# Performance work log

Measured on AMD Instinct MI355X. Metric: run time of the kernel, lower is better.

## Reference

```python
import jax, jax.numpy as jnp
import numpy as np

N_NODES = 100000
N_EDGES = 3200000
IN_DIM = 128
HID = 128
K = 20  # n_gaussians


def gcn_conv(x, src, dst, W, b, n_nodes):
    """PyG GCNConv: add self-loops, symmetric normalization, linear transform.
    out = D^{-1/2} (A + I) D^{-1/2} (x @ W) + b, where D is degree of A+I.
    """
    h = x @ W  # [N, out_dim]
    # degree on A + I (self-loop contributes 1 to every node)
    deg = jax.ops.segment_sum(jnp.ones_like(dst, dtype=h.dtype), dst,
                              num_segments=n_nodes) + 1.0
    dis = jax.lax.rsqrt(deg)  # deg >= 1, safe
    norm = dis[src] * dis[dst]  # [E]
    # gather -> scale -> scatter-add (edges), plus self-loop term dis_i^2 * h_i
    agg = jax.ops.segment_sum(h[src] * norm[:, None], dst,
                              num_segments=n_nodes)
    agg = agg + h * (dis * dis)[:, None]
    return agg + b


def setup_inputs() -> dict:
    key = jax.random.key(0)
    ks = jax.random.split(key, 12)
    x = jax.random.normal(ks[0], (N_NODES, IN_DIM), dtype=jnp.float32)
    edge_index = jax.random.randint(ks[1], (2, N_EDGES), 0, N_NODES, dtype=jnp.int32)
    s = 1.0 / np.sqrt(HID)
    W1 = jax.random.uniform(ks[2], (IN_DIM, HID), jnp.float32, -s, s)
    b1 = jnp.zeros((HID,), jnp.float32)
    W2 = jax.random.uniform(ks[3], (HID, HID), jnp.float32, -s, s)
    b2 = jnp.zeros((HID,), jnp.float32)
    pi_W = jax.random.uniform(ks[4], (HID, K), jnp.float32, -s, s)
    pi_b = jnp.zeros((K,), jnp.float32)
    mu_W = jax.random.uniform(ks[5], (HID, K), jnp.float32, -s, s)
    mu_b = jnp.zeros((K,), jnp.float32)
    ls_W = jax.random.uniform(ks[6], (HID, K), jnp.float32, -s, s)
    ls_b = jnp.zeros((K,), jnp.float32)
    return {"x": x, "edge_index": edge_index, "W1": W1, "b1": b1,
            "W2": W2, "b2": b2, "pi_W": pi_W, "pi_b": pi_b,
            "mu_W": mu_W, "mu_b": mu_b, "ls_W": ls_W, "ls_b": ls_b}


def reference(x, edge_index, W1, b1, W2, b2, pi_W, pi_b, mu_W, mu_b, ls_W, ls_b):
    src, dst = edge_index[0], edge_index[1]
    n = x.shape[0]
    h = jax.nn.relu(gcn_conv(x, src, dst, W1, b1, n))
    h = jax.nn.relu(gcn_conv(h, src, dst, W2, b2, n))
    pi = jax.nn.softmax(h @ pi_W + pi_b, axis=1)
    mu = h @ mu_W + mu_b
    log_sigma = h @ ls_W + ls_b
    return (pi, mu, log_sigma)
```

## Files before the change

### kernel.cpp

```cpp
#include <hip/hip_runtime.h>
#include <hip/hip_fp16.h>
#include <cstdint>
#include <cstddef>

#define IN_DIM 128
#define HID    128
#define NG     20
#define T      4096
#define MAXB   400

__global__ void zero_ints(int* __restrict__ a, int n) {
  int i = blockIdx.x * blockDim.x + threadIdx.x;
  if (i < n) a[i] = 0;
}

__global__ __launch_bounds__(256) void binsort1(const int* __restrict__ src,
    const int* __restrict__ dst, int* __restrict__ tmp, int* __restrict__ bofs,
    int* __restrict__ bintot, int NBC, int E) {
  __shared__ int lhist[MAXB];
  __shared__ int lscan[512];
  __shared__ int lcur[MAXB];
  __shared__ int sbuf[T];
  int tid = threadIdx.x;
  int tile0 = blockIdx.x * T;
  int m = E - tile0; if (m > T) m = T;

  for (int i = tid; i < NBC; i += 256) lhist[i] = 0;
  __syncthreads();

  int dreg[16];
#pragma unroll
  for (int j = 0; j < 16; ++j) {
    int idx = j * 256 + tid;
    dreg[j] = -1;
    if (idx < m) {
      int d = dst[tile0 + idx];
      dreg[j] = d;
      atomicAdd(&lhist[d >> 8], 1);
    }
  }
  __syncthreads();

  int v0 = (tid < NBC) ? lhist[tid] : 0;
  int v1 = (256 + tid < NBC) ? lhist[256 + tid] : 0;
  lscan[tid] = v0; lscan[256 + tid] = v1;
  __syncthreads();
  for (int o = 1; o < 512; o <<= 1) {
    int a0 = (tid >= o) ? lscan[tid - o] : 0;
    int a1 = (256 + tid >= o) ? lscan[256 + tid - o] : 0;
    __syncthreads();
    lscan[tid] += a0; lscan[256 + tid] += a1;
    __syncthreads();
  }
  if (tid < NBC)       lcur[tid]       = lscan[tid] - v0;
  if (256 + tid < NBC) lcur[256 + tid] = lscan[256 + tid] - v1;
  __syncthreads();

  int ST = NBC + 1;
  for (int i = tid; i < NBC; i += 256) bofs[(size_t)blockIdx.x * ST + i] = lcur[i];
  if (tid == 0) bofs[(size_t)blockIdx.x * ST + NBC] = m;
  for (int i = tid; i < NBC; i += 256)
    if (lhist[i]) atomicAdd(&bintot[i], lhist[i]);
  __syncthreads();

#pragma unroll
  for (int j = 0; j < 16; ++j) {
    int idx = j * 256 + tid;
    if (idx < m) {
      int d = dreg[j];
      int s = src[tile0 + idx];
      int slot = atomicAdd(&lcur[d >> 8], 1);
      sbuf[slot] = ((d & 255) << 17) | s;
    }
  }
  __syncthreads();

  int nv = m >> 2;
  int4* out4 = (int4*)(tmp + tile0);
  const int4* sb4 = (const int4*)sbuf;
  for (int i = tid; i < nv; i += 256) out4[i] = sb4[i];
  for (int i = (nv << 2) + tid; i < m; i += 256) tmp[tile0 + i] = sbuf[i];
}

__global__ __launch_bounds__(512) void binscan(const int* __restrict__ bintot,
                                               int* __restrict__ binbase, int NBC) {
  __shared__ int s[512];
  int tid = threadIdx.x;
  int v = (tid < NBC) ? bintot[tid] : 0;
  s[tid] = v;
  __syncthreads();
  for (int o = 1; o < 512; o <<= 1) {
    int t = (tid >= o) ? s[tid - o] : 0;
    __syncthreads();
    s[tid] += t;
    __syncthreads();
  }
  if (tid < NBC) binbase[tid] = s[tid] - v;
}

__global__ __launch_bounds__(512) void binsort2(const int* __restrict__ tmp,
    const int* __restrict__ bofs, const int* __restrict__ binbase,
    int* __restrict__ csrc, int* __restrict__ cnt, float* __restrict__ dis,
    int* __restrict__ offs, int NBC, int nblk, int N) {
  __shared__ int lcnt[256];
  __shared__ int lsc[256];
  __shared__ int lcur2[256];
  int b = blockIdx.x;
  int tid = threadIdx.x;
  if (tid < 256) lcnt[tid] = 0;
  __syncthreads();
  int ST = NBC + 1;
  for (int r = tid; r < nblk; r += 512) {
    int s = bofs[(size_t)r * ST + b];
    int e2 = bofs[(size_t)r * ST + b + 1];
    int base = r * T;
    for (int k = s; k < e2; ++k)
      atomicAdd(&lcnt[tmp[base + k] >> 17], 1);
  }
  __syncthreads();
  if (tid < 256) lsc[tid] = lcnt[tid];
  __syncthreads();
  for (int o = 1; o < 256; o <<= 1) {
    int t = 0;
    if (tid < 256 && tid >= o) t = lsc[tid - o];
    __syncthreads();
    if (tid < 256) lsc[tid] += t;
    __syncthreads();
  }
  int gbase = binbase[b];
  if (tid < 256) {
    int excl = lsc[tid] - lcnt[tid];
    lcur2[tid] = gbase + excl;
    int node = (b << 8) + tid;
    if (node < N) {
      cnt[node] = lcnt[tid];
      dis[node] = rsqrtf((float)lcnt[tid] + 1.0f);
      offs[node] = gbase + excl;
    }
  }
  __syncthreads();
  for (int r = tid; r < nblk; r += 512) {
    int s = bofs[(size_t)r * ST + b];
    int e2 = bofs[(size_t)r * ST + b + 1];
    int base = r * T;
    for (int k = s; k < e2; ++k) {
      int rec = tmp[base + k];
      int pos = atomicAdd(&lcur2[rec >> 17], 1);
      csrc[pos] = rec & 0x1FFFF;
    }
  }
}

#define MT 64
#define KC 64
__global__ __launch_bounds__(256) void gemm128_f16out(const float* __restrict__ A,
                                                      const float* __restrict__ B,
                                                      __half* __restrict__ C, int M) {
  __shared__ float sA[MT][KC + 4];
  __shared__ float sB[KC][128];
  int tid = threadIdx.x;
  int m0 = blockIdx.x * MT;
  int tr = tid >> 4;
  int tc = tid & 15;
  float acc[4][8];
#pragma unroll
  for (int i = 0; i < 4; ++i)
#pragma unroll
    for (int j = 0; j < 8; ++j) acc[i][j] = 0.f;

  for (int k0 = 0; k0 < 128; k0 += KC) {
#pragma unroll
    for (int q = 0; q < 4; ++q) {
      int idx = q * 256 + tid;
      int r = idx >> 4;
      int kk = (idx & 15) << 2;
      float4 v = make_float4(0.f, 0.f, 0.f, 0.f);
      if (m0 + r < M) v = *(const float4*)(A + (size_t)(m0 + r) * 128 + k0 + kk);
      *(float4*)(&sA[r][kk]) = v;
    }
#pragma unroll
    for (int q = 0; q < 8; ++q) {
      int idx = q * 256 + tid;
      int kk = idx >> 5;
      int nn = (idx & 31) << 2;
      *(float4*)(&sB[kk][nn]) = *(const float4*)(B + (size_t)(k0 + kk) * 128 + nn);
    }
    __syncthreads();
#pragma unroll 2
    for (int k = 0; k < KC; k += 4) {
      float4 a0 = *(const float4*)(&sA[tr][k]);
      float4 a1 = *(const float4*)(&sA[tr + 16][k]);
      float4 a2 = *(const float4*)(&sA[tr + 32][k]);
      float4 a3 = *(const float4*)(&sA[tr + 48][k]);
#pragma unroll
      for (int u = 0; u < 4; ++u) {
        float4 blo = *(const float4*)(&sB[k + u][tc * 4]);
        float4 bhi = *(const float4*)(&sB[k + u][64 + tc * 4]);
        float av[4] = {((const float*)&a0)[u], ((const float*)&a1)[u],
                       ((const float*)&a2)[u], ((const float*)&a3)[u]};
        float bl[8] = {blo.x, blo.y, blo.z, blo.w, bhi.x, bhi.y, bhi.z, bhi.w};
#pragma unroll
        for (int i = 0; i < 4; ++i)
#pragma unroll
          for (int j = 0; j < 8; ++j) acc[i][j] = fmaf(av[i], bl[j], acc[i][j]);
      }
    }
    __syncthreads();
  }
#pragma unroll
  for (int i = 0; i < 4; ++i) {
    int r = m0 + tr + 16 * i;
    if (r < M) {
      __half2 p0 = __floats2half2_rn(acc[i][0], acc[i][1]);
      __half2 p1 = __floats2half2_rn(acc[i][2], acc[i][3]);
      __half2 p2 = __floats2half2_rn(acc[i][4], acc[i][5]);
      __half2 p3 = __floats2half2_rn(acc[i][6], acc[i][7]);
      __half2* dst0 = (__half2*)(C + (size_t)r * 128 + tc * 4);
      __half2* dst1 = (__half2*)(C + (size_t)r * 128 + 64 + tc * 4);
      dst0[0] = p0; dst0[1] = p1;
      dst1[0] = p2; dst1[1] = p3;
    }
  }
}

__global__ __launch_bounds__(256) void agg_kernel(const __half* __restrict__ h,
    const int* __restrict__ csrc,
    const int* __restrict__ offs, const int* __restrict__ cnt,
    const float* __restrict__ dis, const float* __restrict__ bias,
    float* __restrict__ out, int n) {
  int wave = threadIdx.x >> 6;
  int lane = threadIdx.x & 63;
  int i0 = (blockIdx.x * 4 + wave) * 2;
  if (i0 >= n) return;
  int i1 = i0 + 1;
  bool has1 = i1 < n;
  int c = lane * 2;

  int st0 = offs[i0];
  int m0  = cnt[i0];
  float d0 = dis[i0];
  int st1 = 0, m1 = 0;
  float d1 = 0.f;
  if (has1) { st1 = offs[i1]; m1 = cnt[i1]; d1 = dis[i1]; }

  float ax0 = 0.f, ay0 = 0.f, ax1 = 0.f, ay1 = 0.f;
  int mMax = m0 > m1 ? m0 : m1;

  for (int base = 0; base < mMax; base += 64) {
    int mcA = m0 - base; mcA = mcA < 0 ? 0 : (mcA > 64 ? 64 : mcA);
    int mcB = m1 - base; mcB = mcB < 0 ? 0 : (mcB > 64 ? 64 : mcB);
    int mc = mcA > mcB ? mcA : mcB;

    int sA = 0, sB = 0;
    float wA = 0.f, wB = 0.f;
    if (lane < mcA) sA = csrc[st0 + base + lane];
    if (lane < mcB) sB = csrc[st1 + base + lane];
    if (lane < mcA) wA = dis[sA] * d0;
    if (lane < mcB) wB = dis[sB] * d1;

    int j = 0;
    for (; j + 4 <= mc; j += 4) {
      int   a0 = __shfl(sA, j);
      int   a1 = __shfl(sA, j + 1);
      int   a2 = __shfl(sA, j + 2);
      int   a3 = __shfl(sA, j + 3);
      int   b0 = __shfl(sB, j);
      int   b1 = __shfl(sB, j + 1);
      int   b2 = __shfl(sB, j + 2);
      int   b3 = __shfl(sB, j + 3);
      float u0 = __shfl(wA, j);
      float u1 = __shfl(wA, j + 1);
      float u2 = __shfl(wA, j + 2);
      float u3 = __shfl(wA, j + 3);
      float v0 = __shfl(wB, j);
      float v1 = __shfl(wB, j + 1);
      float v2 = __shfl(wB, j + 2);
      float v3 = __shfl(wB, j + 3);
      float2 hA0 = __half22float2(*(const __half2*)(h + ((size_t)a0 << 7) + c));
      float2 hA1 = __half22float2(*(const __half2*)(h + ((size_t)a1 << 7) + c));
      float2 hA2 = __half22float2(*(const __half2*)(h + ((size_t)a2 << 7) + c));
      float2 hA3 = __half22float2(*(const __half2*)(h + ((size_t)a3 << 7) + c));
      float2 hB0 = __half22float2(*(const __half2*)(h + ((size_t)b0 << 7) + c));
      float2 hB1 = __half22float2(*(const __half2*)(h + ((size_t)b1 << 7) + c));
      float2 hB2 = __half22float2(*(const __half2*)(h + ((size_t)b2 << 7) + c));
      float2 hB3 = __half22float2(*(const __half2*)(h + ((size_t)b3 << 7) + c));
      ax0 = fmaf(hA0.x, u0, ax0); ay0 = fmaf(hA0.y, u0, ay0);
      ax0 = fmaf(hA1.x, u1, ax0); ay0 = fmaf(hA1.y, u1, ay0);
      ax0 = fmaf(hA2.x, u2, ax0); ay0 = fmaf(hA2.y, u2, ay0);
      ax0 = fmaf(hA3.x, u3, ax0); ay0 = fmaf(hA3.y, u3, ay0);
      ax1 = fmaf(hB0.x, v0, ax1); ay1 = fmaf(hB0.y, v0, ay1);
      ax1 = fmaf(hB1.x, v1, ax1); ay1 = fmaf(hB1.y, v1, ay1);
      ax1 = fmaf(hB2.x, v2, ax1); ay1 = fmaf(hB2.y, v2, ay1);
      ax1 = fmaf(hB3.x, v3, ax1); ay1 = fmaf(hB3.y, v3, ay1);
    }
    for (; j < mc; ++j) {
      int   a0 = __shfl(sA, j);
      int   b0 = __shfl(sB, j);
      float u0 = __shfl(wA, j);
      float v0 = __shfl(wB, j);
      float2 hA0 = __half22float2(*(const __half2*)(h + ((size_t)a0 << 7) + c));
      float2 hB0 = __half22float2(*(const __half2*)(h + ((size_t)b0 << 7) + c));
      ax0 = fmaf(hA0.x, u0, ax0); ay0 = fmaf(hA0.y, u0, ay0);
      ax1 = fmaf(hB0.x, v0, ax1); ay1 = fmaf(hB0.y, v0, ay1);
    }
  }

  float2 bv = *(const float2*)(bias + c);
  {
    float dd = d0 * d0;
    float2 hs = __half22float2(*(const __half2*)(h + ((size_t)i0 << 7) + c));
    float vx = fmaf(hs.x, dd, ax0) + bv.x;
    float vy = fmaf(hs.y, dd, ay0) + bv.y;
    *(float2*)(out + (size_t)i0 * 128 + c) = make_float2(fmaxf(vx, 0.f), fmaxf(vy, 0.f));
  }
  if (has1) {
    float dd = d1 * d1;
    float2 hs = __half22float2(*(const __half2*)(h + ((size_t)i1 << 7) + c));
    float vx = fmaf(hs.x, dd, ax1) + bv.x;
    float vy = fmaf(hs.y, dd, ay1) + bv.y;
    *(float2*)(out + (size_t)i1 * 128 + c) = make_float2(fmaxf(vx, 0.f), fmaxf(vy, 0.f));
  }
}

__global__ void pack_heads_w(const float* __restrict__ piW, const float* __restrict__ muW,
                             const float* __restrict__ lsW, float* __restrict__ W64) {
  int i = blockIdx.x * 256 + threadIdx.x;
  if (i >= 128 * 64) return;
  int k = i >> 6, j = i & 63;
  float v = 0.f;
  if (j < 20)      v = piW[k * 20 + j];
  else if (j < 40) v = muW[k * 20 + (j - 20)];
  else if (j < 60) v = lsW[k * 20 + (j - 40)];
  W64[i] = v;
}

__global__ __launch_bounds__(256) void gemm_heads(const float* __restrict__ A,
                                                  const float* __restrict__ B,
                                                  float* __restrict__ C, int M) {
  __shared__ float sA[64][KC + 4];
  __shared__ float sB[KC][68];
  int tid = threadIdx.x;
  int m0 = blockIdx.x * 64;
  int tr = tid >> 4;
  int tc = tid & 15;
  float acc[4][4];
#pragma unroll
  for (int i = 0; i < 4; ++i)
#pragma unroll
    for (int j = 0; j < 4; ++j) acc[i][j] = 0.f;

  for (int k0 = 0; k0 < 128; k0 += KC) {
#pragma unroll
    for (int q = 0; q < 4; ++q) {
      int idx = q * 256 + tid;
      int r = idx >> 4;
      int kk = (idx & 15) << 2;
      float4 v = make_float4(0.f, 0.f, 0.f, 0.f);
      if (m0 + r < M) v = *(const float4*)(A + (size_t)(m0 + r) * 128 + k0 + kk);
      *(float4*)(&sA[r][kk]) = v;
    }
#pragma unroll
    for (int q = 0; q < 4; ++q) {
      int idx = q * 256 + tid;
      int kk = idx >> 4;
      int nn = (idx & 15) << 2;
      *(float4*)(&sB[kk][nn]) = *(const float4*)(B + (size_t)(k0 + kk) * 64 + nn);
    }
    __syncthreads();
#pragma unroll 4
    for (int k = 0; k < KC; k += 4) {
      float4 a0 = *(const float4*)(&sA[tr][k]);
      float4 a1 = *(const float4*)(&sA[tr + 16][k]);
      float4 a2 = *(const float4*)(&sA[tr + 32][k]);
      float4 a3 = *(const float4*)(&sA[tr + 48][k]);
#pragma unroll
      for (int u = 0; u < 4; ++u) {
        float4 b = *(const float4*)(&sB[k + u][tc * 4]);
        float av[4] = {((const float*)&a0)[u], ((const float*)&a1)[u],
                       ((const float*)&a2)[u], ((const float*)&a3)[u]};
#pragma unroll
        for (int i = 0; i < 4; ++i) {
          acc[i][0] = fmaf(av[i], b.x, acc[i][0]);
          acc[i][1] = fmaf(av[i], b.y, acc[i][1]);
          acc[i][2] = fmaf(av[i], b.z, acc[i][2]);
          acc[i][3] = fmaf(av[i], b.w, acc[i][3]);
        }
      }
    }
    __syncthreads();
  }
#pragma unroll
  for (int i = 0; i < 4; ++i) {
    int r = m0 + tr + 16 * i;
    if (r < M)
      *(float4*)(C + (size_t)r * 64 + tc * 4) =
          make_float4(acc[i][0], acc[i][1], acc[i][2], acc[i][3]);
  }
}

__global__ __launch_bounds__(256) void heads_post(const float* __restrict__ out60,
    const float* __restrict__ pib, const float* __restrict__ mub,
    const float* __restrict__ lsb, float* __restrict__ out, int n) {
  int wave = threadIdx.x >> 6, lane = threadIdx.x & 63;
  int node = blockIdx.x * 4 + wave;
  if (node >= n) return;
  float v = 0.f;
  if (lane < 60) {
    v = out60[(size_t)node * 64 + lane];
    v += (lane < 20) ? pib[lane] : (lane < 40) ? mub[lane - 20] : lsb[lane - 40];
  }
  float pv = (lane < 20) ? v : -__builtin_inff();
  float mx = pv;
  for (int o = 16; o > 0; o >>= 1) mx = fmaxf(mx, __shfl_down(mx, o, 32));
  mx = __shfl(mx, 0, 32);
  float ev = (lane < 20) ? expf(v - mx) : 0.f;
  float sm = ev;
  for (int o = 16; o > 0; o >>= 1) sm += __shfl_down(sm, o, 32);
  sm = __shfl(sm, 0, 32);

  size_t base = (size_t)n * NG;
  if (lane < 20)      out[(size_t)node * NG + lane] = ev / sm;
  else if (lane < 40) out[base + (size_t)node * NG + (lane - 20)] = v;
  else if (lane < 60) out[2 * base + (size_t)node * NG + (lane - 40)] = v;
}

extern "C" void kernel_launch(void* const* d_in, const int* in_sizes, int n_in,
                              void* d_out, int out_size, void* d_ws, size_t ws_size,
                              hipStream_t stream) {
  const float* x   = (const float*)d_in[0];
  const int*   ei  = (const int*)d_in[1];
  const float* W1  = (const float*)d_in[2];
  const float* b1  = (const float*)d_in[3];
  const float* W2  = (const float*)d_in[4];
  const float* b2  = (const float*)d_in[5];
  const float* piW = (const float*)d_in[6];
  const float* pib = (const float*)d_in[7];
  const float* muW = (const float*)d_in[8];
  const float* mub = (const float*)d_in[9];
  const float* lsW = (const float*)d_in[10];
  const float* lsb = (const float*)d_in[11];
  float* out = (float*)d_out;

  const int N = in_sizes[0] / IN_DIM;
  const int E = in_sizes[1] / 2;
  const int* src = ei;
  const int* dst = ei + E;

  const int NBC  = (N + 255) >> 8;
  const int nblk = (E + T - 1) / T;
  const int ST   = NBC + 1;

  char* p = (char*)d_ws;
  char* regionH = p;                        p += (size_t)N * HID * sizeof(__half);
  __half* h16  = (__half*)regionH;
  float* out60 = (float*)regionH;
  char* regionR = p;
  size_t szR = (size_t)N * HID * sizeof(float);
  size_t szT = (size_t)E * sizeof(int);
  p += (szR > szT ? szR : szT);
  int*   tmp    = (int*)regionR;
  float* bufB   = (float*)regionR;
  int*   csrc   = (int*)p;                  p += (size_t)E * sizeof(int);
  int*   bofs   = (int*)p;                  p += (size_t)nblk * ST * sizeof(int);
  int*   bintot = (int*)p;                  p += (size_t)MAXB * sizeof(int);
  int*   binbase= (int*)p;                  p += (size_t)MAXB * sizeof(int);
  int*   cnt    = (int*)p;                  p += (size_t)N * sizeof(int);
  int*   offs   = (int*)p;                  p += (size_t)N * sizeof(int);
  float* dis    = (float*)p;                p += (size_t)N * sizeof(float);
  float* W64    = (float*)p;                p += (size_t)128 * 64 * sizeof(float);

  zero_ints<<<(NBC + 255) / 256, 256, 0, stream>>>(bintot, NBC);
  binsort1<<<nblk, 256, 0, stream>>>(src, dst, tmp, bofs, bintot, NBC, E);
  binscan<<<1, 512, 0, stream>>>(bintot, binbase, NBC);
  binsort2<<<NBC, 512, 0, stream>>>(tmp, bofs, binbase, csrc, cnt, dis, offs,
                                    NBC, nblk, N);
  pack_heads_w<<<(128 * 64 + 255) / 256, 256, 0, stream>>>(piW, muW, lsW, W64);

  const int NB8 = (N + 7) / 8;

  gemm128_f16out<<<(N + MT - 1) / MT, 256, 0, stream>>>(x, W1, h16, N);
  agg_kernel<<<NB8, 256, 0, stream>>>(h16, csrc, offs, cnt, dis, b1, bufB, N);
  gemm128_f16out<<<(N + MT - 1) / MT, 256, 0, stream>>>(bufB, W2, h16, N);
  agg_kernel<<<NB8, 256, 0, stream>>>(h16, csrc, offs, cnt, dis, b2, bufB, N);

  gemm_heads<<<(N + 63) / 64, 256, 0, stream>>>(bufB, W64, out60, N);
  heads_post<<<(N + 3) / 4, 256, 0, stream>>>(out60, pib, mub, lsb, out, N);
}
```

Baseline: 591.2 us.

## Fuse aggregation with following dense transform and heads epilogue

Layer-1 aggregation now computes the 8 aggregated rows per block into shared memory and immediately multiplies them by W2, writing fp16 h directly, eliminating the fp32 intermediate round trip and a separate GEMM launch. The second aggregation likewise fuses the heads GEMM and softmax/split epilogue, removing two kernels and the out60 buffer. The tradeoff is that the fused GEMMs read W from global/L2 per block with little reuse (8 rows per block, no shared tiling of W), so compute efficiency of the dense part drops.

```diff
diff --git a/kernel.cpp b/kernel.cpp
--- a/kernel.cpp
+++ b/kernel.cpp
@@ -223,29 +223,12 @@
   }
 }
 
-__global__ __launch_bounds__(256) void agg_kernel(const __half* __restrict__ h,
-    const int* __restrict__ csrc,
-    const int* __restrict__ offs, const int* __restrict__ cnt,
-    const float* __restrict__ dis, const float* __restrict__ bias,
-    float* __restrict__ out, int n) {
-  int wave = threadIdx.x >> 6;
+__device__ __forceinline__ void agg_core(const __half* __restrict__ h,
+    const int* __restrict__ csrc, const float* __restrict__ dis,
+    int st0, int m0, float d0, int st1, int m1, float d1, int c,
+    float& ax0, float& ay0, float& ax1, float& ay1) {
   int lane = threadIdx.x & 63;
-  int i0 = (blockIdx.x * 4 + wave) * 2;
-  if (i0 >= n) return;
-  int i1 = i0 + 1;
-  bool has1 = i1 < n;
-  int c = lane * 2;
-
-  int st0 = offs[i0];
-  int m0  = cnt[i0];
-  float d0 = dis[i0];
-  int st1 = 0, m1 = 0;
-  float d1 = 0.f;
-  if (has1) { st1 = offs[i1]; m1 = cnt[i1]; d1 = dis[i1]; }
-
-  float ax0 = 0.f, ay0 = 0.f, ax1 = 0.f, ay1 = 0.f;
   int mMax = m0 > m1 ? m0 : m1;
-
   for (int base = 0; base < mMax; base += 64) {
     int mcA = m0 - base; mcA = mcA < 0 ? 0 : (mcA > 64 ? 64 : mcA);
     int mcB = m1 - base; mcB = mcB < 0 ? 0 : (mcB > 64 ? 64 : mcB);
@@ -304,21 +287,161 @@
       ax1 = fmaf(hB0.x, v0, ax1); ay1 = fmaf(hB0.y, v0, ay1);
     }
   }
-
-  float2 bv = *(const float2*)(bias + c);
+}
+
+__global__ __launch_bounds__(256) void agg_gemm_h(const __half* __restrict__ h,
+    const int* __restrict__ csrc, const int* __restrict__ offs,
+    const int* __restrict__ cnt, const float* __restrict__ dis,
+    const float* __restrict__ bias, const float* __restrict__ W,
+    __half* __restrict__ outH, int n) {
+  __shared__ float sRow[8][128];
+  const int tid = threadIdx.x;
+  const int wave = tid >> 6, lane = tid & 63;
+  const int n0 = blockIdx.x * 8;
+  const int i0 = n0 + wave * 2;
+  const int i1 = i0 + 1;
+  const int c = lane * 2;
+
+  if (i0 < n) {
+    const bool has1 = i1 < n;
+    int st0 = offs[i0];
+    int m0  = cnt[i0];
+    float d0 = dis[i0];
+    int st1 = 0, m1 = 0;
+    float d1 = 0.f;
+    if (has1) { st1 = offs[i1]; m1 = cnt[i1]; d1 = dis[i1]; }
+    float ax0 = 0.f, ay0 = 0.f, ax1 = 0.f, ay1 = 0.f;
+    agg_core(h, csrc, dis, st0, m0, d0, st1, m1, d1, c, ax0, ay0, ax1, ay1);
+
+    float2 bv = *(const float2*)(bias + c);
+    {
+      float dd = d0 * d0;
+      float2 hs = __half22float2(*(const __half2*)(h + ((size_t)i0 << 7) + c));
+      sRow[wave * 2][c]     = fmaxf(fmaf(hs.x, dd, ax0) + bv.x, 0.f);
+      sRow[wave * 2][c + 1] = fmaxf(fmaf(hs.y, dd, ay0) + bv.y, 0.f);
+    }
+    if (has1) {
+      float dd = d1 * d1;
+      float2 hs = __half22float2(*(const __half2*)(h + ((size_t)i1 << 7) + c));
+      sRow[wave * 2 + 1][c]     = fmaxf(fmaf(hs.x, dd, ax1) + bv.x, 0.f);
+      sRow[wave * 2 + 1][c + 1] = fmaxf(fmaf(hs.y, dd, ay1) + bv.y, 0.f);
+    }
+  }
+  __syncthreads();
+
+  const int r = tid >> 5;
+  const int q = tid & 31;
+  float4 acc = make_float4(0.f, 0.f, 0.f, 0.f);
+  const float* wp = W + q * 4;
+#pragma unroll 4
+  for (int k = 0; k < 128; k += 4) {
+    float4 a4 = *(const float4*)(&sRow[r][k]);
+    float4 w0 = *(const float4*)(wp + (size_t)(k + 0) * 128);
+    float4 w1 = *(const float4*)(wp + (size_t)(k + 1) * 128);
+    float4 w2 = *(const float4*)(wp + (size_t)(k + 2) * 128);
+    float4 w3 = *(const float4*)(wp + (size_t)(k + 3) * 128);
+    acc.x = fmaf(a4.x, w0.x, acc.x); acc.y = fmaf(a4.x, w0.y, acc.y);
+    acc.z = fmaf(a4.x, w0.z, acc.z); acc.w = fmaf(a4.x, w0.w, acc.w);
+    acc.x = fmaf(a4.y, w1.x, acc.x); acc.y = fmaf(a4.y, w1.y, acc.y);
+    acc.z = fmaf(a4.y, w1.z, acc.z); acc.w = fmaf(a4.y, w1.w, acc.w);
+    acc.x = fmaf(a4.z, w2.x, acc.x); acc.y = fmaf(a4.z, w2.y, acc.y);
+    acc.z = fmaf(a4.z, w2.z, acc.z); acc.w = fmaf(a4.z, w2.w, acc.w);
+    acc.x = fmaf(a4.w, w3.x, acc.x); acc.y = fmaf(a4.w, w3.y, acc.y);
+    acc.z = fmaf(a4.w, w3.z, acc.z); acc.w = fmaf(a4.w, w3.w, acc.w);
+  }
+  if (n0 + r < n) {
+    __half2 p0 = __floats2half2_rn(acc.x, acc.y);
+    __half2 p1 = __floats2half2_rn(acc.z, acc.w);
+    __half2* dp = (__half2*)(outH + (((size_t)(n0 + r)) << 7) + q * 4);
+    dp[0] = p0; dp[1] = p1;
+  }
+}
+
+__global__ __launch_bounds__(256) void agg_gemm_heads(const __half* __restrict__ h,
+    const int* __restrict__ csrc, const int* __restrict__ offs,
+    const int* __restrict__ cnt, const float* __restrict__ dis,
+    const float* __restrict__ bias, const float* __restrict__ W64,
+    const float* __restrict__ pib, const float* __restrict__ mub,
+    const float* __restrict__ lsb, float* __restrict__ out, int n) {
+  __shared__ float sRow[8][128];
+  __shared__ float sOut[8][64];
+  const int tid = threadIdx.x;
+  const int wave = tid >> 6, lane = tid & 63;
+  const int n0 = blockIdx.x * 8;
+  const int i0 = n0 + wave * 2;
+  const int i1 = i0 + 1;
+  const int c = lane * 2;
+
+  if (i0 < n) {
+    const bool has1 = i1 < n;
+    int st0 = offs[i0];
+    int m0  = cnt[i0];
+    float d0 = dis[i0];
+    int st1 = 0, m1 = 0;
+    float d1 = 0.f;
+    if (has1) { st1 = offs[i1]; m1 = cnt[i1]; d1 = dis[i1]; }
+    float ax0 = 0.f, ay0 = 0.f, ax1 = 0.f, ay1 = 0.f;
+    agg_core(h, csrc, dis, st0, m0, d0, st1, m1, d1, c, ax0, ay0, ax1, ay1);
+
+    float2 bv = *(const float2*)(bias + c);
+    {
+      float dd = d0 * d0;
+      float2 hs = __half22float2(*(const __half2*)(h + ((size_t)i0 << 7) + c));
+      sRow[wave * 2][c]     = fmaxf(fmaf(hs.x, dd, ax0) + bv.x, 0.f);
+      sRow[wave * 2][c + 1] = fmaxf(fmaf(hs.y, dd, ay0) + bv.y, 0.f);
+    }
+    if (has1) {
+      float dd = d1 * d1;
+      float2 hs = __half22float2(*(const __half2*)(h + ((size_t)i1 << 7) + c));
+      sRow[wave * 2 + 1][c]     = fmaxf(fmaf(hs.x, dd, ax1) + bv.x, 0.f);
+      sRow[wave * 2 + 1][c + 1] = fmaxf(fmaf(hs.y, dd, ay1) + bv.y, 0.f);
+    }
+  }
+  __syncthreads();
+
   {
-    float dd = d0 * d0;
-    float2 hs = __half22float2(*(const __half2*)(h + ((size_t)i0 << 7) + c));
-    float vx = fmaf(hs.x, dd, ax0) + bv.x;
-    float vy = fmaf(hs.y, dd, ay0) + bv.y;
-    *(float2*)(out + (size_t)i0 * 128 + c) = make_float2(fmaxf(vx, 0.f), fmaxf(vy, 0.f));
-  }
-  if (has1) {
-    float dd = d1 * d1;
-    float2 hs = __half22float2(*(const __half2*)(h + ((size_t)i1 << 7) + c));
-    float vx = fmaf(hs.x, dd, ax1) + bv.x;
-    float vy = fmaf(hs.y, dd, ay1) + bv.y;
-    *(float2*)(out + (size_t)i1 * 128 + c) = make_float2(fmaxf(vx, 0.f), fmaxf(vy, 0.f));
+    const int r = tid >> 5;
+    const int q = tid & 31;
+    float2 acc = make_float2(0.f, 0.f);
+    const float* wp = W64 + q * 2;
+#pragma unroll 4
+    for (int k = 0; k < 128; k += 4) {
+      float4 a4 = *(const float4*)(&sRow[r][k]);
+      float2 w0 = *(const float2*)(wp + (size_t)(k + 0) * 64);
+      float2 w1 = *(const float2*)(wp + (size_t)(k + 1) * 64);
+      float2 w2 = *(const float2*)(wp + (size_t)(k + 2) * 64);
+      float2 w3 = *(const float2*)(wp + (size_t)(k + 3) * 64);
+      acc.x = fmaf(a4.x, w0.x, acc.x); acc.y = fmaf(a4.x, w0.y, acc.y);
+      acc.x = fmaf(a4.y, w1.x, acc.x); acc.y = fmaf(a4.y, w1.y, acc.y);
+      acc.x = fmaf(a4.z, w2.x, acc.x); acc.y = fmaf(a4.z, w2.y, acc.y);
+      acc.x = fmaf(a4.w, w3.x, acc.x); acc.y = fmaf(a4.w, w3.y, acc.y);
+    }
+    sOut[r][q * 2]     = acc.x;
+    sOut[r][q * 2 + 1] = acc.y;
+  }
+  __syncthreads();
+
+  size_t nb = (size_t)n * NG;
+  for (int t = 0; t < 2; ++t) {
+    int rr = wave * 2 + t;
+    int node = n0 + rr;
+    if (node >= n) break;
+    float v = 0.f;
+    if (lane < 60) {
+      v = sOut[rr][lane];
+      v += (lane < 20) ? pib[lane] : (lane < 40) ? mub[lane - 20] : lsb[lane - 40];
+    }
+    float pv = (lane < 20) ? v : -__builtin_inff();
+    float mx = pv;
+    for (int o = 16; o > 0; o >>= 1) mx = fmaxf(mx, __shfl_down(mx, o, 32));
+    mx = __shfl(mx, 0, 32);
+    float ev = (lane < 20) ? expf(v - mx) : 0.f;
+    float sm = ev;
+    for (int o = 16; o > 0; o >>= 1) sm += __shfl_down(sm, o, 32);
+    sm = __shfl(sm, 0, 32);
+    if (lane < 20)      out[(size_t)node * NG + lane] = ev / sm;
+    else if (lane < 40) out[nb + (size_t)node * NG + (lane - 20)] = v;
+    else if (lane < 60) out[2 * nb + (size_t)node * NG + (lane - 40)] = v;
   }
 }
 
@@ -332,96 +455,6 @@
   else if (j < 40) v = muW[k * 20 + (j - 20)];
   else if (j < 60) v = lsW[k * 20 + (j - 40)];
   W64[i] = v;
-}
-
-__global__ __launch_bounds__(256) void gemm_heads(const float* __restrict__ A,
-                                                  const float* __restrict__ B,
-                                                  float* __restrict__ C, int M) {
-  __shared__ float sA[64][KC + 4];
-  __shared__ float sB[KC][68];
-  int tid = threadIdx.x;
-  int m0 = blockIdx.x * 64;
-  int tr = tid >> 4;
-  int tc = tid & 15;
-  float acc[4][4];
-#pragma unroll
-  for (int i = 0; i < 4; ++i)
-#pragma unroll
-    for (int j = 0; j < 4; ++j) acc[i][j] = 0.f;
-
-  for (int k0 = 0; k0 < 128; k0 += KC) {
-#pragma unroll
-    for (int q = 0; q < 4; ++q) {
-      int idx = q * 256 + tid;
-      int r = idx >> 4;
-      int kk = (idx & 15) << 2;
-      float4 v = make_float4(0.f, 0.f, 0.f, 0.f);
-      if (m0 + r < M) v = *(const float4*)(A + (size_t)(m0 + r) * 128 + k0 + kk);
-      *(float4*)(&sA[r][kk]) = v;
-    }
-#pragma unroll
-    for (int q = 0; q < 4; ++q) {
-      int idx = q * 256 + tid;
-      int kk = idx >> 4;
-      int nn = (idx & 15) << 2;
-      *(float4*)(&sB[kk][nn]) = *(const float4*)(B + (size_t)(k0 + kk) * 64 + nn);
-    }
-    __syncthreads();
-#pragma unroll 4
-    for (int k = 0; k < KC; k += 4) {
-      float4 a0 = *(const float4*)(&sA[tr][k]);
-      float4 a1 = *(const float4*)(&sA[tr + 16][k]);
-      float4 a2 = *(const float4*)(&sA[tr + 32][k]);
-      float4 a3 = *(const float4*)(&sA[tr + 48][k]);
-#pragma unroll
-      for (int u = 0; u < 4; ++u) {
-        float4 b = *(const float4*)(&sB[k + u][tc * 4]);
-        float av[4] = {((const float*)&a0)[u], ((const float*)&a1)[u],
-                       ((const float*)&a2)[u], ((const float*)&a3)[u]};
-#pragma unroll
-        for (int i = 0; i < 4; ++i) {
-          acc[i][0] = fmaf(av[i], b.x, acc[i][0]);
-          acc[i][1] = fmaf(av[i], b.y, acc[i][1]);
-          acc[i][2] = fmaf(av[i], b.z, acc[i][2]);
-          acc[i][3] = fmaf(av[i], b.w, acc[i][3]);
-        }
-      }
-    }
-    __syncthreads();
-  }
-#pragma unroll
-  for (int i = 0; i < 4; ++i) {
-    int r = m0 + tr + 16 * i;
-    if (r < M)
-      *(float4*)(C + (size_t)r * 64 + tc * 4) =
-          make_float4(acc[i][0], acc[i][1], acc[i][2], acc[i][3]);
-  }
-}
-
-__global__ __launch_bounds__(256) void heads_post(const float* __restrict__ out60,
-    const float* __restrict__ pib, const float* __restrict__ mub,
-    const float* __restrict__ lsb, float* __restrict__ out, int n) {
-  int wave = threadIdx.x >> 6, lane = threadIdx.x & 63;
-  int node = blockIdx.x * 4 + wave;
-  if (node >= n) return;
-  float v = 0.f;
-  if (lane < 60) {
-    v = out60[(size_t)node * 64 + lane];
-    v += (lane < 20) ? pib[lane] : (lane < 40) ? mub[lane - 20] : lsb[lane - 40];
-  }
-  float pv = (lane < 20) ? v : -__builtin_inff();
-  float mx = pv;
-  for (int o = 16; o > 0; o >>= 1) mx = fmaxf(mx, __shfl_down(mx, o, 32));
-  mx = __shfl(mx, 0, 32);
-  float ev = (lane < 20) ? expf(v - mx) : 0.f;
-  float sm = ev;
-  for (int o = 16; o > 0; o >>= 1) sm += __shfl_down(sm, o, 32);
-  sm = __shfl(sm, 0, 32);
-
-  size_t base = (size_t)n * NG;
-  if (lane < 20)      out[(size_t)node * NG + lane] = ev / sm;
-  else if (lane < 40) out[base + (size_t)node * NG + (lane - 20)] = v;
-  else if (lane < 60) out[2 * base + (size_t)node * NG + (lane - 40)] = v;
 }
 
 extern "C" void kernel_launch(void* const* d_in, const int* in_sizes, int n_in,
@@ -453,13 +486,12 @@
   char* p = (char*)d_ws;
   char* regionH = p;                        p += (size_t)N * HID * sizeof(__half);
   __half* h16  = (__half*)regionH;
-  float* out60 = (float*)regionH;
   char* regionR = p;
   size_t szR = (size_t)N * HID * sizeof(float);
   size_t szT = (size_t)E * sizeof(int);
   p += (szR > szT ? szR : szT);
-  int*   tmp    = (int*)regionR;
-  float* bufB   = (float*)regionR;
+  int*    tmp  = (int*)regionR;
+  __half* h16b = (__half*)regionR;
   int*   csrc   = (int*)p;                  p += (size_t)E * sizeof(int);
   int*   bofs   = (int*)p;                  p += (size_t)nblk * ST * sizeof(int);
   int*   bintot = (int*)p;                  p += (size_t)MAXB * sizeof(int);
@@ -479,10 +511,7 @@
   const int NB8 = (N + 7) / 8;
 
   gemm128_f16out<<<(N + MT - 1) / MT, 256, 0, stream>>>(x, W1, h16, N);
-  agg_kernel<<<NB8, 256, 0, stream>>>(h16, csrc, offs, cnt, dis, b1, bufB, N);
-  gemm128_f16out<<<(N + MT - 1) / MT, 256, 0, stream>>>(bufB, W2, h16, N);
-  agg_kernel<<<NB8, 256, 0, stream>>>(h16, csrc, offs, cnt, dis, b2, bufB, N);
-
-  gemm_heads<<<(N + 63) / 64, 256, 0, stream>>>(bufB, W64, out60, N);
-  heads_post<<<(N + 3) / 4, 256, 0, stream>>>(out60, pib, mub, lsb, out, N);
-}
+  agg_gemm_h<<<NB8, 256, 0, stream>>>(h16, csrc, offs, cnt, dis, b1, W2, h16b, N);
+  agg_gemm_heads<<<NB8, 256, 0, stream>>>(h16b, csrc, offs, cnt, dis, b2, W64,
+                                          pib, mub, lsb, out, N);
+}
```

Result: slower. 725.8 us (+22.8%).

## Replace FP32 SIMT GEMM with FP16 MFMA matrix-core GEMM for 128-wide layers

Applied to the files above, without the earlier changes.

The two 128x128 feature transforms move from a scalar FMA shared-memory tiled GEMM to an MFMA 16x16x32 f16 kernel. The kernel converts A rows to half in LDS, keeps B fragments in registers and uses 128-row tiles. Inputs are now rounded to fp16 before multiply, which may affect accuracy. Output stores become scalar half writes with a strided pattern, and each block re-reads W from global memory with strided loads.

```diff
diff --git a/kernel.cpp b/kernel.cpp
--- a/kernel.cpp
+++ b/kernel.cpp
@@ -8,6 +8,10 @@
 #define NG     20
 #define T      4096
 #define MAXB   400
+
+typedef _Float16 half8 __attribute__((ext_vector_type(8)));
+typedef _Float16 half4 __attribute__((ext_vector_type(4)));
+typedef float    f32x4 __attribute__((ext_vector_type(4)));
 
 __global__ void zero_ints(int* __restrict__ a, int n) {
   int i = blockIdx.x * blockDim.x + threadIdx.x;
@@ -151,74 +155,80 @@
   }
 }
 
-#define MT 64
-#define KC 64
-__global__ __launch_bounds__(256) void gemm128_f16out(const float* __restrict__ A,
-                                                      const float* __restrict__ B,
-                                                      __half* __restrict__ C, int M) {
-  __shared__ float sA[MT][KC + 4];
-  __shared__ float sB[KC][128];
-  int tid = threadIdx.x;
-  int m0 = blockIdx.x * MT;
-  int tr = tid >> 4;
-  int tc = tid & 15;
-  float acc[4][8];
-#pragma unroll
-  for (int i = 0; i < 4; ++i)
-#pragma unroll
-    for (int j = 0; j < 8; ++j) acc[i][j] = 0.f;
-
-  for (int k0 = 0; k0 < 128; k0 += KC) {
-#pragma unroll
-    for (int q = 0; q < 4; ++q) {
-      int idx = q * 256 + tid;
-      int r = idx >> 4;
-      int kk = (idx & 15) << 2;
-      float4 v = make_float4(0.f, 0.f, 0.f, 0.f);
-      if (m0 + r < M) v = *(const float4*)(A + (size_t)(m0 + r) * 128 + k0 + kk);
-      *(float4*)(&sA[r][kk]) = v;
-    }
-#pragma unroll
-    for (int q = 0; q < 8; ++q) {
-      int idx = q * 256 + tid;
-      int kk = idx >> 5;
-      int nn = (idx & 31) << 2;
-      *(float4*)(&sB[kk][nn]) = *(const float4*)(B + (size_t)(k0 + kk) * 128 + nn);
-    }
-    __syncthreads();
-#pragma unroll 2
-    for (int k = 0; k < KC; k += 4) {
-      float4 a0 = *(const float4*)(&sA[tr][k]);
-      float4 a1 = *(const float4*)(&sA[tr + 16][k]);
-      float4 a2 = *(const float4*)(&sA[tr + 32][k]);
-      float4 a3 = *(const float4*)(&sA[tr + 48][k]);
-#pragma unroll
-      for (int u = 0; u < 4; ++u) {
-        float4 blo = *(const float4*)(&sB[k + u][tc * 4]);
-        float4 bhi = *(const float4*)(&sB[k + u][64 + tc * 4]);
-        float av[4] = {((const float*)&a0)[u], ((const float*)&a1)[u],
-                       ((const float*)&a2)[u], ((const float*)&a3)[u]};
-        float bl[8] = {blo.x, blo.y, blo.z, blo.w, bhi.x, bhi.y, bhi.z, bhi.w};
-#pragma unroll
-        for (int i = 0; i < 4; ++i)
-#pragma unroll
-          for (int j = 0; j < 8; ++j) acc[i][j] = fmaf(av[i], bl[j], acc[i][j]);
+__global__ __launch_bounds__(256) void gemm128_mfma(const float* __restrict__ A,
+                                                    const float* __restrict__ B,
+                                                    __half* __restrict__ C, int M) {
+  __shared__ _Float16 sA[128][136];
+  const int tid = threadIdx.x;
+  const int m0 = blockIdx.x * 128;
+
+#pragma unroll
+  for (int q = 0; q < 16; ++q) {
+    int idx = q * 256 + tid;
+    int r = idx >> 5;
+    int cc = (idx & 31) << 2;
+    float4 v = make_float4(0.f, 0.f, 0.f, 0.f);
+    if (m0 + r < M) v = *(const float4*)(A + (size_t)(m0 + r) * 128 + cc);
+    half4 hv;
+    hv[0] = (_Float16)v.x; hv[1] = (_Float16)v.y;
+    hv[2] = (_Float16)v.z; hv[3] = (_Float16)v.w;
+    *(half4*)(&sA[r][cc]) = hv;
+  }
+  __syncthreads();
+
+  const int wave = tid >> 6, lane = tid & 63;
+  const int nbase = wave << 5;
+  const int lrow = lane & 15;
+  const int khi  = lane >> 4;
+
+  half8 bf[2][4];
+#pragma unroll
+  for (int nf = 0; nf < 2; ++nf) {
+    const float* wcol = B + (nbase + nf * 16 + lrow);
+#pragma unroll
+    for (int ks = 0; ks < 4; ++ks) {
+      half8 hb;
+#pragma unroll
+      for (int rr = 0; rr < 8; ++rr)
+        hb[rr] = (_Float16)wcol[(size_t)(ks * 32 + khi * 8 + rr) * 128];
+      bf[nf][ks] = hb;
+    }
+  }
+
+  f32x4 acc[8][2];
+#pragma unroll
+  for (int mf = 0; mf < 8; ++mf)
+#pragma unroll
+    for (int nf = 0; nf < 2; ++nf) acc[mf][nf] = (f32x4){0.f, 0.f, 0.f, 0.f};
+
+#pragma unroll
+  for (int mf = 0; mf < 8; ++mf) {
+    const _Float16* ar = &sA[mf * 16 + lrow][khi * 8];
+    half8 a0 = *(const half8*)(ar);
+    half8 a1 = *(const half8*)(ar + 32);
+    half8 a2 = *(const half8*)(ar + 64);
+    half8 a3 = *(const half8*)(ar + 96);
+    acc[mf][0] = __builtin_amdgcn_mfma_f32_16x16x32_f16(a0, bf[0][0], acc[mf][0], 0, 0, 0);
+    acc[mf][1] = __builtin_amdgcn_mfma_f32_16x16x32_f16(a0, bf[1][0], acc[mf][1], 0, 0, 0);
+    acc[mf][0] = __builtin_amdgcn_mfma_f32_16x16x32_f16(a1, bf[0][1], acc[mf][0], 0, 0, 0);
+    acc[mf][1] = __builtin_amdgcn_mfma_f32_16x16x32_f16(a1, bf[1][1], acc[mf][1], 0, 0, 0);
+    acc[mf][0] = __builtin_amdgcn_mfma_f32_16x16x32_f16(a2, bf[0][2], acc[mf][0], 0, 0, 0);
+    acc[mf][1] = __builtin_amdgcn_mfma_f32_16x16x32_f16(a2, bf[1][2], acc[mf][1], 0, 0, 0);
+    acc[mf][0] = __builtin_amdgcn_mfma_f32_16x16x32_f16(a3, bf[0][3], acc[mf][0], 0, 0, 0);
+    acc[mf][1] = __builtin_amdgcn_mfma_f32_16x16x32_f16(a3, bf[1][3], acc[mf][1], 0, 0, 0);
+  }
+
+#pragma unroll
+  for (int mf = 0; mf < 8; ++mf) {
+    int r0 = mf * 16 + khi * 4;
+#pragma unroll
+    for (int nf = 0; nf < 2; ++nf) {
+      int ccol = nbase + nf * 16 + lrow;
+#pragma unroll
+      for (int reg = 0; reg < 4; ++reg) {
+        int r = m0 + r0 + reg;
+        if (r < M) C[(size_t)r * 128 + ccol] = __float2half(acc[mf][nf][reg]);
       }
-    }
-    __syncthreads();
-  }
-#pragma unroll
-  for (int i = 0; i < 4; ++i) {
-    int r = m0 + tr + 16 * i;
-    if (r < M) {
-      __half2 p0 = __floats2half2_rn(acc[i][0], acc[i][1]);
-      __half2 p1 = __floats2half2_rn(acc[i][2], acc[i][3]);
-      __half2 p2 = __floats2half2_rn(acc[i][4], acc[i][5]);
-      __half2 p3 = __floats2half2_rn(acc[i][6], acc[i][7]);
-      __half2* dst0 = (__half2*)(C + (size_t)r * 128 + tc * 4);
-      __half2* dst1 = (__half2*)(C + (size_t)r * 128 + 64 + tc * 4);
-      dst0[0] = p0; dst0[1] = p1;
-      dst1[0] = p2; dst1[1] = p3;
     }
   }
 }
@@ -334,6 +344,7 @@
   W64[i] = v;
 }
 
+#define KC 64
 __global__ __launch_bounds__(256) void gemm_heads(const float* __restrict__ A,
                                                   const float* __restrict__ B,
                                                   float* __restrict__ C, int M) {
@@ -476,11 +487,12 @@
                                     NBC, nblk, N);
   pack_heads_w<<<(128 * 64 + 255) / 256, 256, 0, stream>>>(piW, muW, lsW, W64);
 
-  const int NB8 = (N + 7) / 8;
-
-  gemm128_f16out<<<(N + MT - 1) / MT, 256, 0, stream>>>(x, W1, h16, N);
+  const int NB8  = (N + 7) / 8;
+  const int NBG  = (N + 127) / 128;
+
+  gemm128_mfma<<<NBG, 256, 0, stream>>>(x, W1, h16, N);
   agg_kernel<<<NB8, 256, 0, stream>>>(h16, csrc, offs, cnt, dis, b1, bufB, N);
-  gemm128_f16out<<<(N + MT - 1) / MT, 256, 0, stream>>>(bufB, W2, h16, N);
+  gemm128_mfma<<<NBG, 256, 0, stream>>>(bufB, W2, h16, N);
   agg_kernel<<<NB8, 256, 0, stream>>>(h16, csrc, offs, cnt, dis, b2, bufB, N);
 
   gemm_heads<<<(N + 63) / 64, 256, 0, stream>>>(bufB, W64, out60, N);
```

Measured after the change: 548.9 us. 7.2% less time.
